# Kernel optimization log

Measured on AMD Instinct MI355X. Metric: run time of the kernel, lower is better.

Reference implementation:

```python
import jax, jax.numpy as jnp
import numpy as np

N, D, H, DH, DFF, E = 4096, 512, 8, 64, 2048, 65536


def setup_inputs() -> dict:
    key = jax.random.key(0)
    ks = jax.random.split(key, 20)
    g = lambda k, s: jax.random.normal(k, s, dtype=jnp.float32) * 0.02
    inp = {
        'x': jax.random.normal(ks[0], (N, D), dtype=jnp.float32),
        'edge_index': jax.random.randint(ks[1], (2, E), 0, N),
        'edge_attr': jax.random.uniform(ks[2], (E,), dtype=jnp.float32),
        'Wg': g(ks[3], (D, D)), 'bg': jnp.zeros((D,), jnp.float32),
        'ln1_s': jnp.ones((D,), jnp.float32), 'ln1_b': jnp.zeros((D,), jnp.float32),
        'Wq': g(ks[4], (D, D)), 'bq': jnp.zeros((D,), jnp.float32),
        'Wk': g(ks[5], (D, D)), 'bk': jnp.zeros((D,), jnp.float32),
        'Wv': g(ks[6], (D, D)), 'bv': jnp.zeros((D,), jnp.float32),
        'Wo': g(ks[7], (D, D)), 'bo': jnp.zeros((D,), jnp.float32),
        'ln2_s': jnp.ones((D,), jnp.float32), 'ln2_b': jnp.zeros((D,), jnp.float32),
        'W1': g(ks[8], (D, DFF)), 'b1': jnp.zeros((DFF,), jnp.float32),
        'W2': g(ks[9], (DFF, D)), 'b2': jnp.zeros((D,), jnp.float32),
        'Wa': g(ks[10], (2 * D, D)), 'ba': jnp.zeros((D,), jnp.float32),
    }
    return inp


def _ln(x, s, b):
    m = x.mean(-1, keepdims=True)
    v = ((x - m) ** 2).mean(-1, keepdims=True)
    return (x - m) * jax.lax.rsqrt(v + 1e-5) * s + b


def _gcn(x, edge_index, ew, Wg, bg):
    # GCNConv: linear, add self-loops (weight 1), sym deg normalization, scatter-add
    xt = x @ Wg                                   # [N, D]
    src = jnp.concatenate([edge_index[0], jnp.arange(N)])
    dst = jnp.concatenate([edge_index[1], jnp.arange(N)])
    w = jnp.concatenate([ew, jnp.ones((N,), ew.dtype)])
    deg = jax.ops.segment_sum(w, dst, num_segments=N)
    dinv = jnp.where(deg > 0, jax.lax.rsqrt(jnp.maximum(deg, 1e-12)), 0.0)
    coef = dinv[src] * w * dinv[dst]              # [E+N]
    out = jax.ops.segment_sum(xt[src] * coef[:, None], dst, num_segments=N)
    return out + bg


def _tfm(x, p):
    # pre-LN vanilla transformer block over all N nodes as one sequence
    h = _ln(x, p['ln1_s'], p['ln1_b'])
    q = (h @ p['Wq'] + p['bq']).reshape(N, H, DH)
    k = (h @ p['Wk'] + p['bk']).reshape(N, H, DH)
    v = (h @ p['Wv'] + p['bv']).reshape(N, H, DH)
    scores = jnp.einsum('nhd,mhd->hnm', q, k) / np.sqrt(DH)
    a = jax.nn.softmax(scores, axis=-1)
    o = jnp.einsum('hnm,mhd->nhd', a, v).reshape(N, D)
    x = x + o @ p['Wo'] + p['bo']
    h2 = _ln(x, p['ln2_s'], p['ln2_b'])
    mlp = jax.nn.gelu(h2 @ p['W1'] + p['b1']) @ p['W2'] + p['b2']
    return x + mlp


def reference(x, edge_index, edge_attr, Wg, bg, ln1_s, ln1_b, Wq, bq, Wk, bk, Wv, bv,
              Wo, bo, ln2_s, ln2_b, W1, b1, W2, b2, Wa, ba):
    p = dict(ln1_s=ln1_s, ln1_b=ln1_b, Wq=Wq, bq=bq, Wk=Wk, bk=bk, Wv=Wv, bv=bv,
             Wo=Wo, bo=bo, ln2_s=ln2_s, ln2_b=ln2_b, W1=W1, b1=b1, W2=W2, b2=b2)
    mp = _gcn(x, edge_index, edge_attr, Wg, bg)
    tf = _tfm(x, p)
    return x + jnp.concatenate([mp, tf], axis=-1) @ Wa + ba
```

## Files before the change

### kernel.cpp

```cpp
#include <hip/hip_runtime.h>
#include <math.h>

#define N_NODES 4096
#define DMODEL  512
#define NHEAD   8
#define DHEAD   64
#define DFF     2048
#define NEDGE   65536
#define QKVLD   1536

typedef unsigned short u16;
typedef __bf16 bf16x8 __attribute__((ext_vector_type(8)));
typedef float  f32x4  __attribute__((ext_vector_type(4)));
typedef short  s16x4  __attribute__((ext_vector_type(4)));

#if defined(__has_builtin)
#if __has_builtin(__builtin_amdgcn_mfma_f32_16x16x16bf16_1k)
#define HAS_MFMA_1K 1
#endif
#endif

__device__ inline float fast_exp2(float x) {
    return __builtin_amdgcn_exp2f(x);
}

__device__ inline f32x4 mfma16(bf16x8 a, bf16x8 b, f32x4 c) {
    return __builtin_amdgcn_mfma_f32_16x16x32_bf16(a, b, c, 0, 0, 0);
}

__device__ inline u16 f2bf(float f) {
    union { float f; unsigned u; } v; v.f = f;
    unsigned r = v.u + 0x7fff + ((v.u >> 16) & 1);
    return (u16)(r >> 16);
}

#ifdef HAS_MFMA_1K
__device__ inline f32x4 mfma1k(s16x4 a, s16x4 b, f32x4 c) {
    return __builtin_amdgcn_mfma_f32_16x16x16bf16_1k(a, b, c, 0, 0, 0);
}
__device__ inline s16x4 pack_bf4(f32x4 p) {
    union { float f; unsigned u; } a0, a1, a2, a3;
    a0.f = p[0]; a1.f = p[1]; a2.f = p[2]; a3.f = p[3];
    unsigned lo = __builtin_amdgcn_perm(a1.u + 0x8000u, a0.u + 0x8000u, 0x07060302u);
    unsigned hi = __builtin_amdgcn_perm(a3.u + 0x8000u, a2.u + 0x8000u, 0x07060302u);
    union { unsigned u[2]; s16x4 v; } r;
    r.u[0] = lo; r.u[1] = hi;
    return r.v;
}
#else
__device__ inline f32x4 mfma1k(s16x4 a, s16x4 b, f32x4 c) { return c; }
__device__ inline s16x4 pack_bf4(f32x4 p) {
    union { u16 u[4]; s16x4 v; } r;
    r.u[0] = f2bf(p[0]); r.u[1] = f2bf(p[1]); r.u[2] = f2bf(p[2]); r.u[3] = f2bf(p[3]);
    return r.v;
}
#endif

__device__ inline float bf2f(u16 v) {
    union { unsigned u; float f; } t; t.u = ((unsigned)v) << 16; return t.f;
}

__device__ inline float gelu_tanh(float x) {
    float x3 = x * x * x;
    float t = tanhf(0.7978845608028654f * (x + 0.044715f * x3));
    return 0.5f * x * (1.0f + t);
}

#define GBN 128
#define GBK 32
#define GP  40

template <int ACT, int OBF16>
__launch_bounds__(512)
__global__ void mfma_gemm64(const u16* __restrict__ A, const u16* __restrict__ Bt,
                            const float* __restrict__ bias, const float* __restrict__ res,
                            void* __restrict__ Cout, int M, int Nn, int K, float scale,
                            int ldC, int ldRes) {
    __shared__ u16 Asm[2][64 * GP];
    __shared__ u16 Bsm[2][128 * GP];

    const int tid = threadIdx.x;
    const int w = tid >> 6;
    const int lane = tid & 63;
    const int quad = lane >> 4;
    const int l15 = lane & 15;
    const int row0 = blockIdx.y * 64;
    const int col0 = blockIdx.x * GBN;
    const int rh = (w & 1) * 32;
    const int cg = (w >> 1) * 32;

    f32x4 acc[2][2];
#pragma unroll
    for (int i = 0; i < 2; ++i)
#pragma unroll
        for (int j = 0; j < 2; ++j) acc[i][j] = (f32x4){0.f, 0.f, 0.f, 0.f};

    const int brow = tid >> 2, bk = (tid & 3) * 8;
    const int arow = (tid & 255) >> 2, ak = (tid & 3) * 8;
    const bool doA = (tid < 256);

    {
        uint4 b0 = *(const uint4*)&Bt[(size_t)(col0 + brow) * K + bk];
        *(uint4*)&Bsm[0][brow * GP + bk] = b0;
        if (doA) {
            uint4 a0 = *(const uint4*)&A[(size_t)(row0 + arow) * K + ak];
            *(uint4*)&Asm[0][arow * GP + ak] = a0;
        }
    }
    __syncthreads();

    const int nT = K / GBK;
    for (int t = 0; t < nT; ++t) {
        const int buf = t & 1;
        uint4 an, bn;
        if (t + 1 < nT) {
            const int k0 = (t + 1) * GBK;
            bn = *(const uint4*)&Bt[(size_t)(col0 + brow) * K + k0 + bk];
            if (doA) an = *(const uint4*)&A[(size_t)(row0 + arow) * K + k0 + ak];
        }
        bf16x8 af[2], bf[2];
#pragma unroll
        for (int i = 0; i < 2; ++i)
            af[i] = *(const bf16x8*)&Asm[buf][(rh + i * 16 + l15) * GP + quad * 8];
#pragma unroll
        for (int j = 0; j < 2; ++j)
            bf[j] = *(const bf16x8*)&Bsm[buf][(cg + j * 16 + l15) * GP + quad * 8];
#pragma unroll
        for (int i = 0; i < 2; ++i)
#pragma unroll
            for (int j = 0; j < 2; ++j)
                acc[i][j] = mfma16(af[i], bf[j], acc[i][j]);
        if (t + 1 < nT) {
            *(uint4*)&Bsm[buf ^ 1][brow * GP + bk] = bn;
            if (doA) *(uint4*)&Asm[buf ^ 1][arow * GP + ak] = an;
            __syncthreads();
        }
    }

#pragma unroll
    for (int j = 0; j < 2; ++j) {
        const int col = col0 + cg + j * 16 + l15;
        const float bc = bias ? bias[col] : 0.f;
#pragma unroll
        for (int i = 0; i < 2; ++i) {
#pragma unroll
            for (int r = 0; r < 4; ++r) {
                const int row = row0 + rh + i * 16 + quad * 4 + r;
                float o = (acc[i][j][r] + bc) * scale;
                if (ACT == 1) o = gelu_tanh(o);
                if (res) o += res[(size_t)row * ldRes + col];
                if (OBF16)
                    ((u16*)Cout)[(size_t)row * ldC + col] = f2bf(o);
                else
                    ((float*)Cout)[(size_t)row * ldC + col] = o;
            }
        }
    }
}

__device__ inline uint4 reduce4_norm(const u16* b0, const u16* b1, size_t off, float linv) {
    const size_t OFF = (size_t)N_NODES * DMODEL;
    float s[8] = {0.f, 0.f, 0.f, 0.f, 0.f, 0.f, 0.f, 0.f};
    const u16* bs[2] = {b0, b1};
#pragma unroll
    for (int b = 0; b < 2; ++b)
#pragma unroll
        for (int k = 0; k < 2; ++k) {
            uint4 v = *(const uint4*)(bs[b] + k * OFF + off);
            unsigned uu[4] = {v.x, v.y, v.z, v.w};
#pragma unroll
            for (int t = 0; t < 4; ++t) {
                s[2 * t]     += bf2f((u16)(uu[t] & 0xffff));
                s[2 * t + 1] += bf2f((u16)(uu[t] >> 16));
            }
        }
    uint4 r;
    r.x = (unsigned)f2bf(s[0] * linv) | ((unsigned)f2bf(s[1] * linv) << 16);
    r.y = (unsigned)f2bf(s[2] * linv) | ((unsigned)f2bf(s[3] * linv) << 16);
    r.z = (unsigned)f2bf(s[4] * linv) | ((unsigned)f2bf(s[5] * linv) << 16);
    r.w = (unsigned)f2bf(s[6] * linv) | ((unsigned)f2bf(s[7] * linv) << 16);
    return r;
}

__launch_bounds__(512)
__global__ void wo_gemm(const u16* __restrict__ Ob0, const u16* __restrict__ Ob1,
                        const float* __restrict__ lpart, const u16* __restrict__ Bt,
                        const float* __restrict__ bias, const float* __restrict__ res,
                        float* __restrict__ Cout) {
    __shared__ u16 Asm[2][64 * GP];
    __shared__ u16 Bsm[2][128 * GP];

    const int tid = threadIdx.x;
    const int w = tid >> 6;
    const int lane = tid & 63;
    const int quad = lane >> 4;
    const int l15 = lane & 15;
    const int row0 = blockIdx.y * 64;
    const int col0 = blockIdx.x * GBN;
    const int rh = (w & 1) * 32;
    const int cg = (w >> 1) * 32;
    const int K = DMODEL;

    f32x4 acc[2][2];
#pragma unroll
    for (int i = 0; i < 2; ++i)
#pragma unroll
        for (int j = 0; j < 2; ++j) acc[i][j] = (f32x4){0.f, 0.f, 0.f, 0.f};

    const int brow = tid >> 2, bk = (tid & 3) * 8;
    const int arow = (tid & 255) >> 2, ak = (tid & 3) * 8;
    const bool doA = (tid < 256);

    float linv[8];
    if (doA) {
        const float* lr = lpart + (size_t)(row0 + arow) * 32;
        float ls[8] = {0.f, 0.f, 0.f, 0.f, 0.f, 0.f, 0.f, 0.f};
#pragma unroll
        for (int v = 0; v < 8; ++v) {
            float4 q = *(const float4*)&lr[v * 4];
            ls[(v * 4 + 0) & 7] += q.x;
            ls[(v * 4 + 1) & 7] += q.y;
            ls[(v * 4 + 2) & 7] += q.z;
            ls[(v * 4 + 3) & 7] += q.w;
        }
#pragma unroll
        for (int hh = 0; hh < 8; ++hh) linv[hh] = 1.0f / ls[hh];
    }

    {
        uint4 b0 = *(const uint4*)&Bt[(size_t)(col0 + brow) * K + bk];
        *(uint4*)&Bsm[0][brow * GP + bk] = b0;
        if (doA) {
            uint4 a0 = reduce4_norm(Ob0, Ob1,
                                    (size_t)(row0 + arow) * DMODEL + ak, linv[0]);
            *(uint4*)&Asm[0][arow * GP + ak] = a0;
        }
    }
    __syncthreads();

#pragma unroll
    for (int t = 0; t < 16; ++t) {
        const int buf = t & 1;
        uint4 an, bn;
        if (t + 1 < 16) {
            const int k0 = (t + 1) * GBK;
            bn = *(const uint4*)&Bt[(size_t)(col0 + brow) * K + k0 + bk];
            if (doA)
                an = reduce4_norm(Ob0, Ob1,
                                  (size_t)(row0 + arow) * DMODEL + k0 + ak,
                                  linv[(t + 1) >> 1]);
        }
        bf16x8 af[2], bf[2];
#pragma unroll
        for (int i = 0; i < 2; ++i)
            af[i] = *(const bf16x8*)&Asm[buf][(rh + i * 16 + l15) * GP + quad * 8];
#pragma unroll
        for (int j = 0; j < 2; ++j)
            bf[j] = *(const bf16x8*)&Bsm[buf][(cg + j * 16 + l15) * GP + quad * 8];
#pragma unroll
        for (int i = 0; i < 2; ++i)
#pragma unroll
            for (int j = 0; j < 2; ++j)
                acc[i][j] = mfma16(af[i], bf[j], acc[i][j]);
        if (t + 1 < 16) {
            *(uint4*)&Bsm[buf ^ 1][brow * GP + bk] = bn;
            if (doA) *(uint4*)&Asm[buf ^ 1][arow * GP + ak] = an;
            __syncthreads();
        }
    }

#pragma unroll
    for (int j = 0; j < 2; ++j) {
        const int col = col0 + cg + j * 16 + l15;
        const float bc = bias[col];
#pragma unroll
        for (int i = 0; i < 2; ++i) {
#pragma unroll
            for (int r = 0; r < 4; ++r) {
                const int row = row0 + rh + i * 16 + quad * 4 + r;
                Cout[(size_t)row * DMODEL + col] =
                    acc[i][j][r] + bc + res[(size_t)row * DMODEL + col];
            }
        }
    }
}

#define QSCALE 0.1803368801111204f

__launch_bounds__(256)
__global__ void qkvg_gemm(const u16* __restrict__ xb, const u16* __restrict__ hb,
                          const u16* __restrict__ Wall,
                          const float* __restrict__ bq, const float* __restrict__ bk,
                          const float* __restrict__ bv,
                          u16* __restrict__ xtb, u16* __restrict__ qkvb,
                          u16* __restrict__ vtb) {
    __shared__ u16 Asm[2][64 * GP];
    __shared__ u16 Bsm[2][128 * GP];

    const int tid = threadIdx.x;
    const int w = tid >> 6;
    const int lane = tid & 63;
    const int quad = lane >> 4;
    const int l15 = lane & 15;
    const int row0 = blockIdx.y * 64;
    const int col0 = blockIdx.x * GBN;
    const int wn = w * 32;
    const int K = DMODEL;
    const u16* A = (col0 < 512) ? xb : hb;

    f32x4 acc[4][2];
#pragma unroll
    for (int i = 0; i < 4; ++i)
#pragma unroll
        for (int j = 0; j < 2; ++j) acc[i][j] = (f32x4){0.f, 0.f, 0.f, 0.f};

    const int c1 = tid, c2 = tid + 256;
    const int ar1 = c1 >> 2, ak1 = (c1 & 3) * 8;
    const int ar2 = c2 >> 2, ak2 = (c2 & 3) * 8;

    {
        uint4 a0 = *(const uint4*)&A   [(size_t)(row0 + ar1) * K + ak1];
        uint4 b0 = *(const uint4*)&Wall[(size_t)(col0 + ar1) * K + ak1];
        uint4 b1 = *(const uint4*)&Wall[(size_t)(col0 + ar2) * K + ak2];
        *(uint4*)&Asm[0][ar1 * GP + ak1] = a0;
        *(uint4*)&Bsm[0][ar1 * GP + ak1] = b0;
        *(uint4*)&Bsm[0][ar2 * GP + ak2] = b1;
    }
    __syncthreads();

    const int nT = K / GBK;
    for (int t = 0; t < nT; ++t) {
        const int buf = t & 1;
        uint4 an, bn0, bn1;
        if (t + 1 < nT) {
            const int k0 = (t + 1) * GBK;
            an  = *(const uint4*)&A   [(size_t)(row0 + ar1) * K + k0 + ak1];
            bn0 = *(const uint4*)&Wall[(size_t)(col0 + ar1) * K + k0 + ak1];
            bn1 = *(const uint4*)&Wall[(size_t)(col0 + ar2) * K + k0 + ak2];
        }
        bf16x8 af[4], bf[2];
#pragma unroll
        for (int i = 0; i < 4; ++i)
            af[i] = *(const bf16x8*)&Asm[buf][(i * 16 + l15) * GP + quad * 8];
#pragma unroll
        for (int j = 0; j < 2; ++j)
            bf[j] = *(const bf16x8*)&Bsm[buf][(wn + j * 16 + l15) * GP + quad * 8];
#pragma unroll
        for (int i = 0; i < 4; ++i)
#pragma unroll
            for (int j = 0; j < 2; ++j)
                acc[i][j] = mfma16(af[i], bf[j], acc[i][j]);
        if (t + 1 < nT) {
            *(uint4*)&Asm[buf ^ 1][ar1 * GP + ak1] = an;
            *(uint4*)&Bsm[buf ^ 1][ar1 * GP + ak1] = bn0;
            *(uint4*)&Bsm[buf ^ 1][ar2 * GP + ak2] = bn1;
            __syncthreads();
        }
    }

#pragma unroll
    for (int j = 0; j < 2; ++j) {
        const int col = col0 + wn + j * 16 + l15;
        if (col < 512) {
#pragma unroll
            for (int i = 0; i < 4; ++i)
#pragma unroll
                for (int r = 0; r < 4; ++r)
                    xtb[(size_t)(row0 + i * 16 + quad * 4 + r) * 512 + col] =
                        f2bf(acc[i][j][r]);
        } else if (col < 1536) {
            const float bc = (col < 1024) ? bq[col - 512] : bk[col - 1024];
            const float scale = (col < 1024) ? QSCALE : 1.0f;
#pragma unroll
            for (int i = 0; i < 4; ++i)
#pragma unroll
                for (int r = 0; r < 4; ++r)
                    qkvb[(size_t)(row0 + i * 16 + quad * 4 + r) * QKVLD + col - 512] =
                        f2bf((acc[i][j][r] + bc) * scale);
        } else {
            const int hd = col - 1536;
            const float bc = bv[hd];
#pragma unroll
            for (int i = 0; i < 4; ++i) {
                ushort4 pk;
                pk.x = f2bf(acc[i][j][0] + bc);
                pk.y = f2bf(acc[i][j][1] + bc);
                pk.z = f2bf(acc[i][j][2] + bc);
                pk.w = f2bf(acc[i][j][3] + bc);
                *(uint2*)&vtb[(size_t)hd * N_NODES + row0 + i * 16 + quad * 4] =
                    *(uint2*)&pk;
            }
        }
    }
}

__device__ inline float block_sum_256(float v, float* red4) {
#pragma unroll
    for (int o = 32; o > 0; o >>= 1) v += __shfl_down(v, o, 64);
    const int lane = threadIdx.x & 63;
    const int w = threadIdx.x >> 6;
    if (lane == 0) red4[w] = v;
    __syncthreads();
    return red4[0] + red4[1] + red4[2] + red4[3];
}

__launch_bounds__(256)
__global__ void prep_kernel(
    const float* __restrict__ Wg, const float* __restrict__ Wq,
    const float* __restrict__ Wk, const float* __restrict__ Wv,
    const float* __restrict__ Wo, const float* __restrict__ W1,
    const float* __restrict__ W2, const float* __restrict__ Wa,
    u16* __restrict__ Wgt, u16* __restrict__ Wqt, u16* __restrict__ Wkt,
    u16* __restrict__ Wvt, u16* __restrict__ Wot, u16* __restrict__ W1t,
    u16* __restrict__ W2t, u16* __restrict__ Wat,
    const float* __restrict__ x, u16* __restrict__ xb,
    const float* __restrict__ ln1s, const float* __restrict__ ln1b,
    u16* __restrict__ hb, float* __restrict__ deg, int* __restrict__ cnt) {
    __shared__ u16 t[32][34];
    __shared__ float redA[4];
    __shared__ float redB[4];
    const int id = blockIdx.x;

    if (id < 3840) {
        const float* W; u16* Wt; int K, Nn, bx, by;
        if (id < 1280) {
            const int m = id >> 8, tt = id & 255;
            bx = tt & 15; by = tt >> 4; K = 512; Nn = 512;
            W  = (m == 0) ? Wg  : (m == 1) ? Wq  : (m == 2) ? Wk  : (m == 3) ? Wv  : Wo;
            Wt = (m == 0) ? Wgt : (m == 1) ? Wqt : (m == 2) ? Wkt : (m == 3) ? Wvt : Wot;
        } else if (id < 2304) {
            const int tt = id - 1280; bx = tt & 63; by = tt >> 6;
            K = 512; Nn = 2048; W = W1; Wt = W1t;
        } else if (id < 3328) {
            const int tt = id - 2304; bx = tt & 15; by = tt >> 4;
            K = 2048; Nn = 512; W = W2; Wt = W2t;
        } else {
            const int tt = id - 3328; bx = tt & 15; by = tt >> 4;
            K = 1024; Nn = 512; W = Wa; Wt = Wat;
        }
        const int k0 = by * 32, n0 = bx * 32;
        const int r = threadIdx.x >> 3, c4 = (threadIdx.x & 7) * 4;
        float4 v = *(const float4*)&W[(size_t)(k0 + r) * Nn + n0 + c4];
        t[r][c4 + 0] = f2bf(v.x); t[r][c4 + 1] = f2bf(v.y);
        t[r][c4 + 2] = f2bf(v.z); t[r][c4 + 3] = f2bf(v.w);
        __syncthreads();
        u16 tmp[4];
#pragma unroll
        for (int i = 0; i < 4; ++i) tmp[i] = t[c4 + i][r];
        u16* op = Wt + (size_t)(n0 + r) * K + k0 + c4;
        *(uint2*)op = *(uint2*)tmp;
    } else if (id < 7936) {
        const int row = id - 3840;
        const int tid = threadIdx.x;
        const float* xr = x + (size_t)row * DMODEL;
        float v0 = xr[tid], v1 = xr[tid + 256];
        xb[(size_t)row * DMODEL + tid] = f2bf(v0);
        xb[(size_t)row * DMODEL + tid + 256] = f2bf(v1);
        float total = block_sum_256(v0 + v1, redA);
        float mean = total * (1.0f / DMODEL);
        float d0 = v0 - mean, d1 = v1 - mean;
        float sq = block_sum_256(d0 * d0 + d1 * d1, redB);
        float inv = rsqrtf(sq * (1.0f / DMODEL) + 1e-5f);
        hb[(size_t)row * DMODEL + tid] = f2bf(d0 * inv * ln1s[tid] + ln1b[tid]);
        hb[(size_t)row * DMODEL + tid + 256] =
            f2bf(d1 * inv * ln1s[tid + 256] + ln1b[tid + 256]);
    } else {
        int i = (id - 7936) * 256 + threadIdx.x;
        deg[i] = 1.0f;
        cnt[i] = 0;
    }
}

__launch_bounds__(256)
__global__ void ln_kernel(const float* __restrict__ X, const float* __restrict__ s,
                          const float* __restrict__ b, u16* __restrict__ Y) {
    __shared__ float redA[4];
    __shared__ float redB[4];
    const int row = blockIdx.x;
    const int tid = threadIdx.x;
    const float* xr = X + (size_t)row * DMODEL;
    float v0 = xr[tid], v1 = xr[tid + 256];
    float total = block_sum_256(v0 + v1, redA);
    float mean = total * (1.0f / DMODEL);
    float d0 = v0 - mean, d1 = v1 - mean;
    float sq = block_sum_256(d0 * d0 + d1 * d1, redB);
    float inv = rsqrtf(sq * (1.0f / DMODEL) + 1e-5f);
    Y[(size_t)row * DMODEL + tid] = f2bf(d0 * inv * s[tid] + b[tid]);
    Y[(size_t)row * DMODEL + tid + 256] = f2bf(d1 * inv * s[tid + 256] + b[tid + 256]);
}

__global__ void gcn_count_kernel(const int* __restrict__ ei, const float* __restrict__ ew,
                                 float* __restrict__ deg, int* __restrict__ cnt) {
    int e = blockIdx.x * 256 + threadIdx.x;
    int d = ei[NEDGE + e];
    atomicAdd(&cnt[d], 1);
    atomicAdd(&deg[d], ew[e]);
}

__launch_bounds__(256)
__global__ void gcn_prefix_kernel(const int* __restrict__ cnt, int* __restrict__ off,
                                  int* __restrict__ cur, const float* __restrict__ deg,
                                  float* __restrict__ dinv) {
    __shared__ int part[256];
    const int tid = threadIdx.x;
    int local[16];
    int s = 0;
#pragma unroll
    for (int i = 0; i < 16; ++i) { local[i] = s; s += cnt[tid * 16 + i]; }
    part[tid] = s;
#pragma unroll
    for (int i = 0; i < 16; ++i) {
        const int n = tid * 16 + i;
        float d = deg[n];
        dinv[n] = (d > 0.f) ? rsqrtf(fmaxf(d, 1e-12f)) : 0.f;
    }
    __syncthreads();
    if (tid == 0) {
        int run = 0;
        for (int j = 0; j < 256; ++j) { int t = part[j]; part[j] = run; run += t; }
        off[N_NODES] = run;
    }
    __syncthreads();
    int p = part[tid];
#pragma unroll
    for (int i = 0; i < 16; ++i) {
        off[tid * 16 + i] = p + local[i];
        cur[tid * 16 + i] = p + local[i];
    }
}

__global__ void gcn_fill_kernel(const int* __restrict__ ei, const float* __restrict__ ew,
                                int* __restrict__ cur, int* __restrict__ esrc,
                                float* __restrict__ eww) {
    int e = blockIdx.x * 256 + threadIdx.x;
    int s = ei[e], d = ei[NEDGE + e];
    int pos = atomicAdd(&cur[d], 1);
    esrc[pos] = s;
    eww[pos] = ew[e];
}

__launch_bounds__(256)
__global__ void gcn_gather_kernel(const u16* __restrict__ xtb, const int* __restrict__ off,
                                  const int* __restrict__ esrc, const float* __restrict__ eww,
                                  const float* __restrict__ dinv, const float* __restrict__ bg,
                                  u16* __restrict__ catb) {
    const int d = blockIdx.x;
    const int b0 = off[d], b1 = off[d + 1];
    const float did = dinv[d];
    const int c = threadIdx.x * 2;
    float a0 = 0.f, a1 = 0.f;
    for (int j = b0; j < b1; ++j) {
        const int s = esrc[j];
        const float coef = dinv[s] * eww[j] * did;
        const unsigned pv = *(const unsigned*)&xtb[(size_t)s * DMODEL + c];
        a0 += coef * bf2f((u16)(pv & 0xffff));
        a1 += coef * bf2f((u16)(pv >> 16));
    }
    {
        const unsigned pv = *(const unsigned*)&xtb[(size_t)d * DMODEL + c];
        const float sl = did * did;
        a0 += sl * bf2f((u16)(pv & 0xffff));
        a1 += sl * bf2f((u16)(pv >> 16));
    }
    const unsigned pk = (unsigned)f2bf(a0 + bg[c]) | ((unsigned)f2bf(a1 + bg[c + 1]) << 16);
    *(unsigned*)&catb[(size_t)d * 1024 + c] = pk;
}

#define TK 64
#define AP 72
#define NSPLIT 4
#define KSPAN (N_NODES / NSPLIT)
#define TQ 256

__launch_bounds__(256, 2)
__global__ void attn_kernel(const u16* __restrict__ Qkv, const u16* __restrict__ Vtb,
                            u16* __restrict__ Ob0, u16* __restrict__ Ob1,
                            float* __restrict__ lpart) {
    __shared__ u16 Ks[2][64 * AP];
    __shared__ u16 Vs[2][64 * AP];

    const int h = blockIdx.x;
    const int q0 = blockIdx.y * TQ;
    const int sp = blockIdx.z;
    u16* __restrict__ Opx = ((sp < 2) ? Ob0 : Ob1) + (size_t)(sp & 1) * N_NODES * DMODEL;
    const int kbase = sp * KSPAN;

    const int tid = threadIdx.x;
    const int w = tid >> 6;
    const int lane = tid & 63;
    const int quad = lane >> 4;
    const int l15 = lane & 15;

    const u16* qp = Qkv + (size_t)(q0 + w * 64 + l15) * QKVLD + h * DHEAD + quad * 8;
    bf16x8 qf[4][2];
#pragma unroll
    for (int a = 0; a < 4; ++a) {
        qf[a][0] = *(const bf16x8*)(qp + (size_t)a * 16 * QKVLD);
        qf[a][1] = *(const bf16x8*)(qp + (size_t)a * 16 * QKVLD + 32);
    }

    f32x4 Oa[4][4];
#pragma unroll
    for (int a = 0; a < 4; ++a)
#pragma unroll
        for (int g = 0; g < 4; ++g) Oa[a][g] = (f32x4){0.f, 0.f, 0.f, 0.f};
    float ls[4] = {0.f, 0.f, 0.f, 0.f};

    const int srow = (tid & 127) >> 1;
    const int scol = (tid & 1) * 32;
    const bool isK = (tid < 128);

    {
        if (isK) {
            const uint4* kg = (const uint4*)(Qkv + (size_t)(kbase + srow) * QKVLD + 512 + h * DHEAD + scol);
            uint4* kd = (uint4*)&Ks[0][srow * AP + scol];
            kd[0] = kg[0]; kd[1] = kg[1]; kd[2] = kg[2]; kd[3] = kg[3];
        } else {
            const uint4* vg = (const uint4*)(Vtb + ((size_t)h * DHEAD + srow) * N_NODES + kbase + scol);
            uint4* vd = (uint4*)&Vs[0][srow * AP + scol];
            vd[0] = vg[0]; vd[1] = vg[1]; vd[2] = vg[2]; vd[3] = vg[3];
        }
    }
    __syncthreads();

    const int NT = KSPAN / TK;
    for (int t = 0; t < NT; ++t) {
        const int buf = t & 1;
        const bool more = (t + 1 < NT);
        uint4 s0, s1, s2, s3;
        if (more) {
            const int kn = kbase + (t + 1) * TK;
            if (isK) {
                const uint4* kg = (const uint4*)(Qkv + (size_t)(kn + srow) * QKVLD + 512 + h * DHEAD + scol);
                s0 = kg[0]; s1 = kg[1]; s2 = kg[2]; s3 = kg[3];
            } else {
                const uint4* vg = (const uint4*)(Vtb + ((size_t)h * DHEAD + srow) * N_NODES + kn + scol);
                s0 = vg[0]; s1 = vg[1]; s2 = vg[2]; s3 = vg[3];
            }
        }

        bf16x8 kf0[4], kf1[4];
#pragma unroll
        for (int f = 0; f < 4; ++f) {
            const u16* kr = &Ks[buf][(f * 16 + l15) * AP + quad * 8];
            kf0[f] = *(const bf16x8*)kr;
            kf1[f] = *(const bf16x8*)(kr + 32);
        }
        s16x4 vv[4][4];
#pragma unroll
        for (int g = 0; g < 4; ++g)
#pragma unroll
            for (int f = 0; f < 4; ++f)
                vv[f][g] = *(const s16x4*)&Vs[buf][(g * 16 + l15) * AP + f * 16 + quad * 4];

#pragma unroll
        for (int a = 0; a < 4; ++a) {
            f32x4 St[4];
            __builtin_amdgcn_s_setprio(1);
#pragma unroll
            for (int f = 0; f < 4; ++f) {
                f32x4 z = (f32x4){0.f, 0.f, 0.f, 0.f};
                z = mfma16(kf0[f], qf[a][0], z);
                St[f] = mfma16(kf1[f], qf[a][1], z);
            }
            __builtin_amdgcn_s_setprio(0);
            s16x4 pk[4];
#pragma unroll
            for (int f = 0; f < 4; ++f) {
                f32x4 p;
                p[0] = fast_exp2(St[f][0]);
                p[1] = fast_exp2(St[f][1]);
                p[2] = fast_exp2(St[f][2]);
                p[3] = fast_exp2(St[f][3]);
                ls[a] += (p[0] + p[1]) + (p[2] + p[3]);
                pk[f] = pack_bf4(p);
            }
            __builtin_amdgcn_s_setprio(1);
#pragma unroll
            for (int f = 0; f < 4; ++f)
#pragma unroll
                for (int g = 0; g < 4; ++g)
                    Oa[a][g] = mfma1k(pk[f], vv[f][g], Oa[a][g]);
            __builtin_amdgcn_s_setprio(0);
        }

        if (more) {
            if (isK) {
                uint4* kd = (uint4*)&Ks[buf ^ 1][srow * AP + scol];
                kd[0] = s0; kd[1] = s1; kd[2] = s2; kd[3] = s3;
            } else {
                uint4* vd = (uint4*)&Vs[buf ^ 1][srow * AP + scol];
                vd[0] = s0; vd[1] = s1; vd[2] = s2; vd[3] = s3;
            }
            __syncthreads();
        }
    }

#pragma unroll
    for (int a = 0; a < 4; ++a) {
        float s = ls[a];
        s += __shfl_xor(s, 16, 64);
        s += __shfl_xor(s, 32, 64);
        const int rowbase = q0 + w * 64 + a * 16;
        if (quad == 0)
            lpart[(size_t)(rowbase + l15) * 32 + sp * 8 + h] = s;
#pragma unroll
        for (int r = 0; r < 4; ++r) {
            u16* op = Opx + (size_t)(rowbase + quad * 4 + r) * DMODEL + h * DHEAD + l15;
#pragma unroll
            for (int g = 0; g < 4; ++g) op[g * 16] = f2bf(Oa[a][g][r]);
        }
    }
}

static void mgemm64(hipStream_t st, const u16* A, const u16* Bt, const float* bias,
                    const float* res, void* C, int M, int Nn, int K, float scale,
                    int act, int obf16, int ldC, int ldRes) {
    dim3 g(Nn / GBN, M / 64), b(512);
    if (act)
        hipLaunchKernelGGL((mfma_gemm64<1, 1>), g, b, 0, st, A, Bt, bias, res, C, M, Nn, K, scale, ldC, ldRes);
    else if (obf16)
        hipLaunchKernelGGL((mfma_gemm64<0, 1>), g, b, 0, st, A, Bt, bias, res, C, M, Nn, K, scale, ldC, ldRes);
    else
        hipLaunchKernelGGL((mfma_gemm64<0, 0>), g, b, 0, st, A, Bt, bias, res, C, M, Nn, K, scale, ldC, ldRes);
}

extern "C" void kernel_launch(void* const* d_in, const int* in_sizes, int n_in,
                              void* d_out, int out_size, void* d_ws, size_t ws_size,
                              hipStream_t stream) {
    const float* x    = (const float*)d_in[0];
    const int*   ei   = (const int*)d_in[1];
    const float* ew   = (const float*)d_in[2];
    const float* Wg   = (const float*)d_in[3];
    const float* bg   = (const float*)d_in[4];
    const float* ln1s = (const float*)d_in[5];
    const float* ln1b = (const float*)d_in[6];
    const float* Wq   = (const float*)d_in[7];
    const float* bq   = (const float*)d_in[8];
    const float* Wk   = (const float*)d_in[9];
    const float* bk   = (const float*)d_in[10];
    const float* Wv   = (const float*)d_in[11];
    const float* bv   = (const float*)d_in[12];
    const float* Wo   = (const float*)d_in[13];
    const float* bo   = (const float*)d_in[14];
    const float* ln2s = (const float*)d_in[15];
    const float* ln2b = (const float*)d_in[16];
    const float* W1   = (const float*)d_in[17];
    const float* b1   = (const float*)d_in[18];
    const float* W2   = (const float*)d_in[19];
    const float* b2   = (const float*)d_in[20];
    const float* Wa   = (const float*)d_in[21];
    const float* ba   = (const float*)d_in[22];
    float* out = (float*)d_out;
    float* ws  = (float*)d_ws;

    const size_t SLOT = (size_t)N_NODES * DMODEL;

    u16* xtb = (u16*)ws;
    u16* Ob0 = (u16*)ws;
    float* lpart = ws + SLOT;
    int*   esrc  = (int*)(ws + SLOT + 327680);
    float* eww   = (float*)(esrc + NEDGE);
    int*   off   = (int*)(eww + NEDGE);
    int*   cur   = off + 4100;
    int*   cnt   = cur + 4096;
    u16* Ob1 = (u16*)(ws + 2 * SLOT);
    u16* hb  = (u16*)(ws + 3 * SLOT);
    u16* h2b = hb + SLOT;
    u16*   qkvb = (u16*)(ws + 4 * SLOT);
    float* x1   = ws + 4 * SLOT;
    u16*   vtb  = (u16*)(ws + 5 * SLOT) + SLOT;
    u16* midb = (u16*)(ws + 6 * SLOT);
    u16* catb = (u16*)(ws + 8 * SLOT);
    u16* xb   = catb;
    u16* Wgt = (u16*)(ws + 9 * SLOT);
    u16* Wqt = Wgt + 262144;
    u16* Wkt = Wqt + 262144;
    u16* Wvt = Wkt + 262144;
    u16* Wot = Wvt + 262144;
    u16* W1t = Wot + 262144;
    u16* W2t = W1t + 1048576;
    u16* Wat = W2t + 1048576;
    float* deg  = (float*)(Wat + 524288);
    float* dinv = deg + N_NODES;

    hipLaunchKernelGGL(prep_kernel, dim3(7952), dim3(256), 0, stream,
                       Wg, Wq, Wk, Wv, Wo, W1, W2, Wa,
                       Wgt, Wqt, Wkt, Wvt, Wot, W1t, W2t, Wat,
                       x, xb, ln1s, ln1b, hb, deg, cnt);

    hipLaunchKernelGGL(qkvg_gemm, dim3(16, 64), dim3(256), 0, stream,
                       xb, hb, Wgt, bq, bk, bv, xtb, qkvb, vtb);

    hipLaunchKernelGGL(gcn_count_kernel, dim3(NEDGE / 256), dim3(256), 0, stream, ei, ew, deg, cnt);
    hipLaunchKernelGGL(gcn_prefix_kernel, dim3(1), dim3(256), 0, stream, cnt, off, cur, deg, dinv);
    hipLaunchKernelGGL(gcn_fill_kernel, dim3(NEDGE / 256), dim3(256), 0, stream, ei, ew, cur, esrc, eww);
    hipLaunchKernelGGL(gcn_gather_kernel, dim3(N_NODES), dim3(256), 0, stream,
                       xtb, off, esrc, eww, dinv, bg, catb);

    hipLaunchKernelGGL(attn_kernel, dim3(NHEAD, N_NODES / TQ, NSPLIT), dim3(256), 0, stream,
                       qkvb, vtb, Ob0, Ob1, lpart);

    hipLaunchKernelGGL(wo_gemm, dim3(4, 64), dim3(512), 0, stream,
                       Ob0, Ob1, lpart, Wot, bo, x, x1);

    hipLaunchKernelGGL(ln_kernel, dim3(N_NODES), dim3(256), 0, stream, x1, ln2s, ln2b, h2b);
    mgemm64(stream, h2b, W1t, b1, nullptr, midb, N_NODES, DFF, DMODEL, 1.0f, 1, 1, DFF, DFF);
    mgemm64(stream, midb, W2t, b2, x1, catb + 512, N_NODES, DMODEL, DFF, 1.0f, 0, 1, 1024, DMODEL);

    mgemm64(stream, catb, Wat, ba, x, out, N_NODES, DMODEL, 2 * DMODEL, 1.0f, 0, 0, DMODEL, DMODEL);
}
```

Before: 318.2 us.

## Load GEMM tiles directly global-to-LDS with global_load_lds in three GEMMs

```diff
diff --git a/kernel.cpp b/kernel.cpp
--- a/kernel.cpp
+++ b/kernel.cpp
@@ -17,6 +17,9 @@
 #if defined(__has_builtin)
 #if __has_builtin(__builtin_amdgcn_mfma_f32_16x16x16bf16_1k)
 #define HAS_MFMA_1K 1
+#endif
+#if __has_builtin(__builtin_amdgcn_global_load_lds)
+#define HAS_GLOAD_LDS 1
 #endif
 #endif
 
@@ -56,6 +59,16 @@
 }
 #endif
 
+__device__ inline void gld16(const u16* g, u16* l) {
+#ifdef HAS_GLOAD_LDS
+    __builtin_amdgcn_global_load_lds((const __attribute__((address_space(1))) void*)g,
+                                     (__attribute__((address_space(3))) void*)l,
+                                     16, 0, 0);
+#else
+    *(uint4*)l = *(const uint4*)g;
+#endif
+}
+
 __device__ inline float bf2f(u16 v) {
     union { unsigned u; float f; } t; t.u = ((unsigned)v) << 16; return t.f;
 }
@@ -76,8 +89,8 @@
                             const float* __restrict__ bias, const float* __restrict__ res,
                             void* __restrict__ Cout, int M, int Nn, int K, float scale,
                             int ldC, int ldRes) {
-    __shared__ u16 Asm[2][64 * GP];
-    __shared__ u16 Bsm[2][128 * GP];
+    __shared__ u16 Asm[2][64 * 32];
+    __shared__ u16 Bsm[2][128 * 32];
 
     const int tid = threadIdx.x;
     const int w = tid >> 6;
@@ -95,46 +108,38 @@
 #pragma unroll
         for (int j = 0; j < 2; ++j) acc[i][j] = (f32x4){0.f, 0.f, 0.f, 0.f};
 
-    const int brow = tid >> 2, bk = (tid & 3) * 8;
-    const int arow = (tid & 255) >> 2, ak = (tid & 3) * 8;
-    const bool doA = (tid < 256);
-
-    {
-        uint4 b0 = *(const uint4*)&Bt[(size_t)(col0 + brow) * K + bk];
-        *(uint4*)&Bsm[0][brow * GP + bk] = b0;
-        if (doA) {
-            uint4 a0 = *(const uint4*)&A[(size_t)(row0 + arow) * K + ak];
-            *(uint4*)&Asm[0][arow * GP + ak] = a0;
-        }
-    }
+    const int crow = lane >> 2;
+    const int ck = (lane & 3) * 8;
+    const u16* gB = &Bt[(size_t)(col0 + w * 16 + crow) * K + ck];
+    const u16* gA = &A [(size_t)(row0 + (w & 3) * 16 + crow) * K + ck];
+    const int lBo = w * 512;
+    const int lAo = (w & 3) * 512;
+
+    gld16(gB, &Bsm[0][lBo]);
+    if (w < 4) gld16(gA, &Asm[0][lAo]);
     __syncthreads();
 
     const int nT = K / GBK;
     for (int t = 0; t < nT; ++t) {
         const int buf = t & 1;
-        uint4 an, bn;
         if (t + 1 < nT) {
             const int k0 = (t + 1) * GBK;
-            bn = *(const uint4*)&Bt[(size_t)(col0 + brow) * K + k0 + bk];
-            if (doA) an = *(const uint4*)&A[(size_t)(row0 + arow) * K + k0 + ak];
+            gld16(gB + k0, &Bsm[buf ^ 1][lBo]);
+            if (w < 4) gld16(gA + k0, &Asm[buf ^ 1][lAo]);
         }
         bf16x8 af[2], bf[2];
 #pragma unroll
         for (int i = 0; i < 2; ++i)
-            af[i] = *(const bf16x8*)&Asm[buf][(rh + i * 16 + l15) * GP + quad * 8];
+            af[i] = *(const bf16x8*)&Asm[buf][(rh + i * 16 + l15) * 32 + quad * 8];
 #pragma unroll
         for (int j = 0; j < 2; ++j)
-            bf[j] = *(const bf16x8*)&Bsm[buf][(cg + j * 16 + l15) * GP + quad * 8];
+            bf[j] = *(const bf16x8*)&Bsm[buf][(cg + j * 16 + l15) * 32 + quad * 8];
 #pragma unroll
         for (int i = 0; i < 2; ++i)
 #pragma unroll
             for (int j = 0; j < 2; ++j)
                 acc[i][j] = mfma16(af[i], bf[j], acc[i][j]);
-        if (t + 1 < nT) {
-            *(uint4*)&Bsm[buf ^ 1][brow * GP + bk] = bn;
-            if (doA) *(uint4*)&Asm[buf ^ 1][arow * GP + ak] = an;
-            __syncthreads();
-        }
+        if (t + 1 < nT) __syncthreads();
     }
 
 #pragma unroll
@@ -188,7 +193,7 @@
                         const float* __restrict__ bias, const float* __restrict__ res,
                         float* __restrict__ Cout) {
     __shared__ u16 Asm[2][64 * GP];
-    __shared__ u16 Bsm[2][128 * GP];
+    __shared__ u16 Bsm[2][128 * 32];
 
     const int tid = threadIdx.x;
     const int w = tid >> 6;
@@ -207,7 +212,11 @@
 #pragma unroll
         for (int j = 0; j < 2; ++j) acc[i][j] = (f32x4){0.f, 0.f, 0.f, 0.f};
 
-    const int brow = tid >> 2, bk = (tid & 3) * 8;
+    const int crow = lane >> 2;
+    const int ck = (lane & 3) * 8;
+    const u16* gB = &Bt[(size_t)(col0 + w * 16 + crow) * K + ck];
+    const int lBo = w * 512;
+
     const int arow = (tid & 255) >> 2, ak = (tid & 3) * 8;
     const bool doA = (tid < 256);
 
@@ -228,11 +237,9 @@
     }
 
     {
-        uint4 b0 = *(const uint4*)&Bt[(size_t)(col0 + brow) * K + bk];
-        *(uint4*)&Bsm[0][brow * GP + bk] = b0;
+        gld16(gB, &Bsm[0][lBo]);
         if (doA) {
-            uint4 a0 = reduce4_norm(Ob0, Ob1,
-                                    (size_t)(row0 + arow) * DMODEL + ak, linv[0]);
+            uint4 a0 = reduce4_norm(Ob0, Ob1, (size_t)(row0 + arow) * DMODEL + ak, linv[0]);
             *(uint4*)&Asm[0][arow * GP + ak] = a0;
         }
     }
@@ -241,13 +248,12 @@
 #pragma unroll
     for (int t = 0; t < 16; ++t) {
         const int buf = t & 1;
-        uint4 an, bn;
+        uint4 an;
         if (t + 1 < 16) {
             const int k0 = (t + 1) * GBK;
-            bn = *(const uint4*)&Bt[(size_t)(col0 + brow) * K + k0 + bk];
+            gld16(gB + k0, &Bsm[buf ^ 1][lBo]);
             if (doA)
-                an = reduce4_norm(Ob0, Ob1,
-                                  (size_t)(row0 + arow) * DMODEL + k0 + ak,
+                an = reduce4_norm(Ob0, Ob1, (size_t)(row0 + arow) * DMODEL + k0 + ak,
                                   linv[(t + 1) >> 1]);
         }
         bf16x8 af[2], bf[2];
@@ -256,14 +262,13 @@
             af[i] = *(const bf16x8*)&Asm[buf][(rh + i * 16 + l15) * GP + quad * 8];
 #pragma unroll
         for (int j = 0; j < 2; ++j)
-            bf[j] = *(const bf16x8*)&Bsm[buf][(cg + j * 16 + l15) * GP + quad * 8];
+            bf[j] = *(const bf16x8*)&Bsm[buf][(cg + j * 16 + l15) * 32 + quad * 8];
 #pragma unroll
         for (int i = 0; i < 2; ++i)
 #pragma unroll
             for (int j = 0; j < 2; ++j)
                 acc[i][j] = mfma16(af[i], bf[j], acc[i][j]);
         if (t + 1 < 16) {
-            *(uint4*)&Bsm[buf ^ 1][brow * GP + bk] = bn;
             if (doA) *(uint4*)&Asm[buf ^ 1][arow * GP + ak] = an;
             __syncthreads();
         }
@@ -294,8 +299,8 @@
                           const float* __restrict__ bv,
                           u16* __restrict__ xtb, u16* __restrict__ qkvb,
                           u16* __restrict__ vtb) {
-    __shared__ u16 Asm[2][64 * GP];
-    __shared__ u16 Bsm[2][128 * GP];
+    __shared__ u16 Asm[2][64 * 32];
+    __shared__ u16 Bsm[2][128 * 32];
 
     const int tid = threadIdx.x;
     const int w = tid >> 6;
@@ -314,48 +319,44 @@
 #pragma unroll
         for (int j = 0; j < 2; ++j) acc[i][j] = (f32x4){0.f, 0.f, 0.f, 0.f};
 
-    const int c1 = tid, c2 = tid + 256;
-    const int ar1 = c1 >> 2, ak1 = (c1 & 3) * 8;
-    const int ar2 = c2 >> 2, ak2 = (c2 & 3) * 8;
+    const int crow = lane >> 2;
+    const int ck = (lane & 3) * 8;
+    const u16* gA  = &A   [(size_t)(row0 + w * 16 + crow) * K + ck];
+    const u16* gB0 = &Wall[(size_t)(col0 + w * 32 + crow) * K + ck];
+    const u16* gB1 = &Wall[(size_t)(col0 + w * 32 + 16 + crow) * K + ck];
+    const int lAo = w * 512;
+    const int lB0 = w * 1024;
+    const int lB1 = w * 1024 + 512;
 
     {
-        uint4 a0 = *(const uint4*)&A   [(size_t)(row0 + ar1) * K + ak1];
-        uint4 b0 = *(const uint4*)&Wall[(size_t)(col0 + ar1) * K + ak1];
-        uint4 b1 = *(const uint4*)&Wall[(size_t)(col0 + ar2) * K + ak2];
-        *(uint4*)&Asm[0][ar1 * GP + ak1] = a0;
-        *(uint4*)&Bsm[0][ar1 * GP + ak1] = b0;
-        *(uint4*)&Bsm[0][ar2 * GP + ak2] = b1;
+        gld16(gA, &Asm[0][lAo]);
+        gld16(gB0, &Bsm[0][lB0]);
+        gld16(gB1, &Bsm[0][lB1]);
     }
     __syncthreads();
 
     const int nT = K / GBK;
     for (int t = 0; t < nT; ++t) {
         const int buf = t & 1;
-        uint4 an, bn0, bn1;
         if (t + 1 < nT) {
             const int k0 = (t + 1) * GBK;
-            an  = *(const uint4*)&A   [(size_t)(row0 + ar1) * K + k0 + ak1];
-            bn0 = *(const uint4*)&Wall[(size_t)(col0 + ar1) * K + k0 + ak1];
-            bn1 = *(const uint4*)&Wall[(size_t)(col0 + ar2) * K + k0 + ak2];
+            gld16(gA + k0, &Asm[buf ^ 1][lAo]);
+            gld16(gB0 + k0, &Bsm[buf ^ 1][lB0]);
+            gld16(gB1 + k0, &Bsm[buf ^ 1][lB1]);
         }
         bf16x8 af[4], bf[2];
 #pragma unroll
         for (int i = 0; i < 4; ++i)
-            af[i] = *(const bf16x8*)&Asm[buf][(i * 16 + l15) * GP + quad * 8];
+            af[i] = *(const bf16x8*)&Asm[buf][(i * 16 + l15) * 32 + quad * 8];
 #pragma unroll
         for (int j = 0; j < 2; ++j)
-            bf[j] = *(const bf16x8*)&Bsm[buf][(wn + j * 16 + l15) * GP + quad * 8];
+            bf[j] = *(const bf16x8*)&Bsm[buf][(wn + j * 16 + l15) * 32 + quad * 8];
 #pragma unroll
         for (int i = 0; i < 4; ++i)
 #pragma unroll
             for (int j = 0; j < 2; ++j)
                 acc[i][j] = mfma16(af[i], bf[j], acc[i][j]);
-        if (t + 1 < nT) {
-            *(uint4*)&Asm[buf ^ 1][ar1 * GP + ak1] = an;
-            *(uint4*)&Bsm[buf ^ 1][ar1 * GP + ak1] = bn0;
-            *(uint4*)&Bsm[buf ^ 1][ar2 * GP + ak2] = bn1;
-            __syncthreads();
-        }
+        if (t + 1 < nT) __syncthreads();
     }
 
 #pragma unroll
```

Result: no change. 316.8 us (-0.5%).
